# Kernel tuning notes

Measured on AMD Instinct MI355X. Metric: run time of the kernel, lower is better.

The kernel has to match this reference:

```python
import jax, jax.numpy as jnp
import numpy as np


def setup_inputs() -> dict:
    key = jax.random.key(0)
    ks = jax.random.split(key, 5)
    B, T, in_dim, out_dim = 8, 1024, 4096, 4096
    b_in, b_out, bs_in, bs_out, rank = 16, 16, 256, 256, 128
    std = np.sqrt(0.02).astype(np.float32)
    x = jax.random.normal(ks[0], (B, T, in_dim), dtype=jnp.float32)
    S = jax.random.uniform(ks[1], (b_out, b_in, rank), dtype=jnp.float32)
    U = std * jax.random.normal(ks[2], (b_out, rank, bs_out), dtype=jnp.float32)
    Vt = std * jax.random.normal(ks[3], (b_in, bs_in, rank), dtype=jnp.float32)
    bias = jax.random.normal(ks[4], (out_dim,), dtype=jnp.float32)
    return {"x": x, "S": S, "U": U, "Vt": Vt, "bias": bias}


def _blast_weight(S, U, Vt, in_dim):
    # Faithful to AbstractBlast.weight(eye(in_dim)): pass identity through the
    # block low-rank chain to materialize the dense weight W (in_dim, out_dim).
    b_in, bs_in, rank = Vt.shape
    I = jnp.eye(in_dim, dtype=Vt.dtype)
    # xp: (b_in, in_dim, bs_in) -- block-column slices of the identity
    xp = I.reshape(in_dim, b_in, bs_in).transpose(1, 0, 2)
    y = jnp.einsum('jms,jsr->jmr', xp, Vt)     # (b_in, in_dim, rank)
    z = jnp.einsum('jmr,ojr->omr', y, S)        # (b_out, in_dim, rank)
    out = jnp.einsum('omr,orp->omp', z, U)      # (b_out, in_dim, bs_out)
    W = out.transpose(1, 0, 2).reshape(in_dim, -1)  # (in_dim, out_dim)
    return W


def reference(x, S, U, Vt, bias):
    in_dim = x.shape[-1]
    X = x.reshape(-1, in_dim)                   # to2D
    W = _blast_weight(S, U, Vt, in_dim)
    out = bias + X @ W                          # addmm
    return out.reshape(*x.shape[:-1], -1)       # undo_to2D
```

## Files before the change

kernel.cpp:

```cpp
#include <hip/hip_runtime.h>
#include <hip/hip_bf16.h>


typedef __bf16 bf16x8 __attribute__((ext_vector_type(8)));
typedef __bf16 bf16x4 __attribute__((ext_vector_type(4)));
typedef float  f32x4  __attribute__((ext_vector_type(4)));

#define IN_DIM  4096
#define OUT_DIM 4096
#define NROWS   8192
#define BJ      16
#define BO      16
#define RANK    128

__device__ __forceinline__ bf16x4 cvt4(f32x4 v) {
  bf16x4 r;
  r[0] = (__bf16)v[0]; r[1] = (__bf16)v[1]; r[2] = (__bf16)v[2]; r[3] = (__bf16)v[3];
  return r;
}
__device__ __forceinline__ f32x4 lo4(bf16x8 v) {
  return (f32x4){(float)v[0], (float)v[1], (float)v[2], (float)v[3]};
}
__device__ __forceinline__ f32x4 hi4(bf16x8 v) {
  return (f32x4){(float)v[4], (float)v[5], (float)v[6], (float)v[7]};
}

__global__ __launch_bounds__(256) void prep_frag(
    const float* __restrict__ Vt, const float* __restrict__ U,
    __bf16* __restrict__ vtf, __bf16* __restrict__ utf)
{
  const int NV = BJ * 256 * RANK;
  int v = blockIdx.x * 256 + threadIdx.x;
  if (v < NV) {
    const int e = v & 7, lane = (v >> 3) & 63, ks = (v >> 9) & 7,
              rf = (v >> 12) & 7, j = v >> 15;
    const int l = lane & 15, lh = lane >> 4;
    const int s = ks * 32 + lh * 8 + e, r = rf * 16 + l;
    vtf[v] = (__bf16)Vt[((size_t)(j * 256 + s)) * RANK + r];
  } else {
    const int u = v - NV;
    const int e = u & 7, lane = (u >> 3) & 63, ks = (u >> 9) & 3,
              pf = (u >> 11) & 15, o = u >> 15;
    const int l = lane & 15, lh = lane >> 4;
    const int r = ks * 32 + lh * 8 + e, p = pf * 16 + l;
    utf[u] = (__bf16)U[((size_t)(o * RANK + r)) * 256 + p];
  }
}

__global__ __launch_bounds__(256, 4) void k1_T(
    const float* __restrict__ x, const __bf16* __restrict__ vtf,
    __bf16* __restrict__ T)
{
  __shared__ __bf16 X_lds[64 * 256];

  const int tid  = threadIdx.x;
  const int lane = tid & 63;
  const int w    = tid >> 6;
  const int l15  = lane & 15;
  const int lhi  = lane >> 4;
  const int b    = blockIdx.x;
  const int j    = (b >> 3) & 15;
  const int mt   = (b & 7) * 16 + (b >> 7);
  const size_t rowbase = (size_t)mt * 64;

  #pragma unroll
  for (int i = 0; i < 16; ++i) {
    const int row = w * 16 + i;
    const f32x4 v = __builtin_nontemporal_load(
        (const f32x4*)(x + (rowbase + row) * IN_DIM + j * 256 + lane * 4));
    const int c = (lane >> 1) ^ (row & 15);
    *(bf16x4*)&X_lds[row * 256 + c * 8 + (lane & 1) * 4] = cvt4(v);
  }
  __syncthreads();

  f32x4 acc[2][4];
  #pragma unroll
  for (int a = 0; a < 2; ++a)
    #pragma unroll
    for (int c = 0; c < 4; ++c) acc[a][c] = (f32x4){0.f, 0.f, 0.f, 0.f};

  const __bf16* va = vtf + ((size_t)(j * 8 + w * 2) * 8) * 512 + lane * 8;
  #pragma unroll
  for (int ks = 0; ks < 8; ++ks) {
    bf16x8 bfr[4];
    #pragma unroll
    for (int nf = 0; nf < 4; ++nf) {
      const int c = (ks * 4 + lhi) ^ l15;
      bfr[nf] = *(const bf16x8*)&X_lds[(nf * 16 + l15) * 256 + c * 8];
    }
    const bf16x8 a0 = *(const bf16x8*)(va + (size_t)ks * 512);
    const bf16x8 a1 = *(const bf16x8*)(va + (size_t)(8 + ks) * 512);
    #pragma unroll
    for (int nf = 0; nf < 4; ++nf) {
      acc[0][nf] = __builtin_amdgcn_mfma_f32_16x16x32_bf16(a0, bfr[nf], acc[0][nf], 0, 0, 0);
      acc[1][nf] = __builtin_amdgcn_mfma_f32_16x16x32_bf16(a1, bfr[nf], acc[1][nf], 0, 0, 0);
    }
  }
  #pragma unroll
  for (int rfi = 0; rfi < 2; ++rfi)
    #pragma unroll
    for (int nf = 0; nf < 4; ++nf) {
      *(bf16x4*)&T[((size_t)j * NROWS + rowbase + nf * 16 + l15) * RANK
                   + (w * 2 + rfi) * 16 + lhi * 4] = cvt4(acc[rfi][nf]);
    }
}

__global__ __launch_bounds__(256, 4) void k2_fused(
    const __bf16* __restrict__ T, const float* __restrict__ S,
    const __bf16* __restrict__ utf, const float* __restrict__ bias,
    float* __restrict__ out)
{
  __shared__ float  S_lds[BJ * RANK];
  __shared__ __bf16 u_lds[64 * RANK];

  const int tid = threadIdx.x;
  const int b   = blockIdx.x;
  const int o   = (b >> 3) & 15;
  const int mt  = (b & 7) * 16 + (b >> 7);
  const size_t rowbase = (size_t)mt * 64;

  {
    const float* sb = S + (size_t)o * (BJ * RANK);
    #pragma unroll
    for (int h = 0; h < 2; ++h) {
      const int idx = tid + h * 256;
      *(f32x4*)&S_lds[idx * 4] = *(const f32x4*)(sb + idx * 4);
    }
  }
  __syncthreads();

  {
    const int nb = tid >> 4;
    const int rs = tid & 15;
    const __bf16* tg = T + (rowbase + nb * 4) * RANK + rs * 8;
    const size_t jstride = (size_t)NROWS * RANK;
    f32x4 uac[4][2];
    #pragma unroll
    for (int i = 0; i < 4; ++i) {
      uac[i][0] = (f32x4){0.f, 0.f, 0.f, 0.f};
      uac[i][1] = (f32x4){0.f, 0.f, 0.f, 0.f};
    }

    #pragma unroll 4
    for (int jb = 0; jb < BJ; ++jb) {
      const __bf16* tj = tg + (size_t)jb * jstride;
      bf16x8 tv[4];
      #pragma unroll
      for (int i = 0; i < 4; ++i) tv[i] = *(const bf16x8*)(tj + i * RANK);
      const float* sj = &S_lds[jb * RANK + rs * 8];
      const f32x4 s0 = *(const f32x4*)(sj);
      const f32x4 s1 = *(const f32x4*)(sj + 4);
      #pragma unroll
      for (int i = 0; i < 4; ++i) {
        uac[i][0] = s0 * lo4(tv[i]) + uac[i][0];
        uac[i][1] = s1 * hi4(tv[i]) + uac[i][1];
      }
    }
    #pragma unroll
    for (int i = 0; i < 4; ++i) {
      const int n = nb * 4 + i;
      bf16x8 uw;
      const f32x4 a = uac[i][0], bb = uac[i][1];
      uw[0]=(__bf16)a[0];  uw[1]=(__bf16)a[1];  uw[2]=(__bf16)a[2];  uw[3]=(__bf16)a[3];
      uw[4]=(__bf16)bb[0]; uw[5]=(__bf16)bb[1]; uw[6]=(__bf16)bb[2]; uw[7]=(__bf16)bb[3];
      const int swz = rs ^ (n & 15);
      *(bf16x8*)&u_lds[n * RANK + swz * 8] = uw;
    }
  }
  __syncthreads();

  {
    const int lane = tid & 63;
    const int w    = tid >> 6;
    const int l15  = lane & 15;
    const int lhi  = lane >> 4;

    f32x4 acc[4][4];
    #pragma unroll
    for (int a = 0; a < 4; ++a)
      #pragma unroll
      for (int c = 0; c < 4; ++c) acc[a][c] = (f32x4){0.f, 0.f, 0.f, 0.f};

    #pragma unroll
    for (int ks = 0; ks < 4; ++ks) {
      bf16x8 ubf[4];
      #pragma unroll
      for (int nf = 0; nf < 4; ++nf) {
        const int swz = (ks * 4 + lhi) ^ l15;
        ubf[nf] = *(const bf16x8*)&u_lds[(nf * 16 + l15) * RANK + swz * 8];
      }
      #pragma unroll
      for (int pi = 0; pi < 4; ++pi) {
        const bf16x8 af = *(const bf16x8*)(
            utf + ((size_t)((o * 16 + w * 4 + pi) * 4 + ks)) * 512 + lane * 8);
        #pragma unroll
        for (int nf = 0; nf < 4; ++nf)
          acc[pi][nf] = __builtin_amdgcn_mfma_f32_16x16x32_bf16(af, ubf[nf], acc[pi][nf], 0, 0, 0);
      }
    }

    #pragma unroll
    for (int pi = 0; pi < 4; ++pi) {
      const int colb = o * 256 + (w * 4 + pi) * 16 + lhi * 4;
      const f32x4 bv = *(const f32x4*)(bias + colb);
      #pragma unroll
      for (int nf = 0; nf < 4; ++nf) {
        __builtin_nontemporal_store(acc[pi][nf] + bv,
            (f32x4*)(out + (rowbase + nf * 16 + l15) * OUT_DIM + colb));
      }
    }
  }
}

extern "C" void kernel_launch(void* const* d_in, const int* in_sizes, int n_in,
                              void* d_out, int out_size, void* d_ws, size_t ws_size,
                              hipStream_t stream) {
  const float* x    = (const float*)d_in[0];
  const float* S    = (const float*)d_in[1];
  const float* U    = (const float*)d_in[2];
  const float* Vt   = (const float*)d_in[3];
  const float* bias = (const float*)d_in[4];
  float* out = (float*)d_out;

  __bf16* vtf = (__bf16*)d_ws;
  __bf16* utf = vtf + (size_t)BJ * 8 * 8 * 512;
  __bf16* T   = utf + (size_t)BO * 16 * 4 * 512;

  prep_frag<<<(2 * 524288) / 256, 256, 0, stream>>>(Vt, U, vtf, utf);
  k1_T<<<(NROWS / 64) * BJ, 256, 0, stream>>>(x, vtf, T);
  k2_fused<<<(NROWS / 64) * BO, 256, 0, stream>>>(T, S, utf, bias, out);
}
```

Baseline: 99.66 us.

## Transpose weight fragments through LDS and read S directly from global

The single scalar-gather prep kernel is split into two kernels, one for Vt and one for U. Each stages a coalesced float4 tile in padded shared memory and writes bf16x8 MFMA fragments, replacing the strided per-element global reads. The fused second kernel now reads S straight from global memory instead of staging it in LDS. That drops one barrier and 8KB of LDS per block, at the cost of repeated global or cache reads of S.

Measured after the change: 103.7 us. 1.04x slower.

```diff
diff --git a/kernel.cpp b/kernel.cpp
--- a/kernel.cpp
+++ b/kernel.cpp
@@ -25,25 +25,69 @@
   return (f32x4){(float)v[4], (float)v[5], (float)v[6], (float)v[7]};
 }
 
-__global__ __launch_bounds__(256) void prep_frag(
-    const float* __restrict__ Vt, const float* __restrict__ U,
-    __bf16* __restrict__ vtf, __bf16* __restrict__ utf)
-{
-  const int NV = BJ * 256 * RANK;
-  int v = blockIdx.x * 256 + threadIdx.x;
-  if (v < NV) {
-    const int e = v & 7, lane = (v >> 3) & 63, ks = (v >> 9) & 7,
-              rf = (v >> 12) & 7, j = v >> 15;
-    const int l = lane & 15, lh = lane >> 4;
-    const int s = ks * 32 + lh * 8 + e, r = rf * 16 + l;
-    vtf[v] = (__bf16)Vt[((size_t)(j * 256 + s)) * RANK + r];
-  } else {
-    const int u = v - NV;
-    const int e = u & 7, lane = (u >> 3) & 63, ks = (u >> 9) & 3,
-              pf = (u >> 11) & 15, o = u >> 15;
-    const int l = lane & 15, lh = lane >> 4;
-    const int r = ks * 32 + lh * 8 + e, p = pf * 16 + l;
-    utf[u] = (__bf16)U[((size_t)(o * RANK + r)) * 256 + p];
+__global__ __launch_bounds__(256) void prep_vtf(
+    const float* __restrict__ Vt, __bf16* __restrict__ vtf)
+{
+  __shared__ float t[32 * 129];
+  const int tid = threadIdx.x;
+  const int j   = blockIdx.x >> 3;
+  const int ks  = blockIdx.x & 7;
+
+  #pragma unroll
+  for (int it = 0; it < 4; ++it) {
+    const int c  = tid + it * 256;
+    const int sr = c >> 5, r4 = c & 31;
+    const f32x4 v = *(const f32x4*)(Vt + ((size_t)(j * 256 + ks * 32 + sr)) * RANK + r4 * 4);
+    t[sr * 129 + r4 * 4 + 0] = v[0];
+    t[sr * 129 + r4 * 4 + 1] = v[1];
+    t[sr * 129 + r4 * 4 + 2] = v[2];
+    t[sr * 129 + r4 * 4 + 3] = v[3];
+  }
+  __syncthreads();
+
+  const int lane = tid & 63;
+  const int l = lane & 15, lh = lane >> 4;
+  #pragma unroll
+  for (int h = 0; h < 2; ++h) {
+    const int rf = (tid >> 6) + h * 4;
+    bf16x8 o8;
+    #pragma unroll
+    for (int e = 0; e < 8; ++e)
+      o8[e] = (__bf16)t[(lh * 8 + e) * 129 + rf * 16 + l];
+    *(bf16x8*)&vtf[(((size_t)(j * 8 + rf) * 8 + ks) * 64 + lane) * 8] = o8;
+  }
+}
+
+__global__ __launch_bounds__(256) void prep_utf(
+    const float* __restrict__ U, __bf16* __restrict__ utf)
+{
+  __shared__ float t[32 * 257];
+  const int tid = threadIdx.x;
+  const int o   = blockIdx.x >> 2;
+  const int ks  = blockIdx.x & 3;
+
+  #pragma unroll
+  for (int it = 0; it < 8; ++it) {
+    const int c  = tid + it * 256;
+    const int rr = c >> 6, p4 = c & 63;
+    const f32x4 v = *(const f32x4*)(U + ((size_t)(o * RANK + ks * 32 + rr)) * 256 + p4 * 4);
+    t[rr * 257 + p4 * 4 + 0] = v[0];
+    t[rr * 257 + p4 * 4 + 1] = v[1];
+    t[rr * 257 + p4 * 4 + 2] = v[2];
+    t[rr * 257 + p4 * 4 + 3] = v[3];
+  }
+  __syncthreads();
+
+  const int lane = tid & 63;
+  const int l = lane & 15, lh = lane >> 4;
+  #pragma unroll
+  for (int h = 0; h < 4; ++h) {
+    const int pf = (tid >> 6) + h * 4;
+    bf16x8 o8;
+    #pragma unroll
+    for (int e = 0; e < 8; ++e)
+      o8[e] = (__bf16)t[(lh * 8 + e) * 257 + pf * 16 + l];
+    *(bf16x8*)&utf[(((size_t)(o * 16 + pf) * 4 + ks) * 64 + lane) * 8] = o8;
   }
 }
 
@@ -110,7 +154,6 @@
     const __bf16* __restrict__ utf, const float* __restrict__ bias,
     float* __restrict__ out)
 {
-  __shared__ float  S_lds[BJ * RANK];
   __shared__ __bf16 u_lds[64 * RANK];
 
   const int tid = threadIdx.x;
@@ -120,19 +163,10 @@
   const size_t rowbase = (size_t)mt * 64;
 
   {
-    const float* sb = S + (size_t)o * (BJ * RANK);
-    #pragma unroll
-    for (int h = 0; h < 2; ++h) {
-      const int idx = tid + h * 256;
-      *(f32x4*)&S_lds[idx * 4] = *(const f32x4*)(sb + idx * 4);
-    }
-  }
-  __syncthreads();
-
-  {
     const int nb = tid >> 4;
     const int rs = tid & 15;
     const __bf16* tg = T + (rowbase + nb * 4) * RANK + rs * 8;
+    const float*  sp = S + (size_t)o * (BJ * RANK) + rs * 8;
     const size_t jstride = (size_t)NROWS * RANK;
     f32x4 uac[4][2];
     #pragma unroll
@@ -147,9 +181,8 @@
       bf16x8 tv[4];
       #pragma unroll
       for (int i = 0; i < 4; ++i) tv[i] = *(const bf16x8*)(tj + i * RANK);
-      const float* sj = &S_lds[jb * RANK + rs * 8];
-      const f32x4 s0 = *(const f32x4*)(sj);
-      const f32x4 s1 = *(const f32x4*)(sj + 4);
+      const f32x4 s0 = *(const f32x4*)(sp + jb * RANK);
+      const f32x4 s1 = *(const f32x4*)(sp + jb * RANK + 4);
       #pragma unroll
       for (int i = 0; i < 4; ++i) {
         uac[i][0] = s0 * lo4(tv[i]) + uac[i][0];
@@ -226,7 +259,8 @@
   __bf16* utf = vtf + (size_t)BJ * 8 * 8 * 512;
   __bf16* T   = utf + (size_t)BO * 16 * 4 * 512;
 
-  prep_frag<<<(2 * 524288) / 256, 256, 0, stream>>>(Vt, U, vtf, utf);
+  prep_vtf<<<BJ * 8, 256, 0, stream>>>(Vt, vtf);
+  prep_utf<<<BO * 4, 256, 0, stream>>>(U, utf);
   k1_T<<<(NROWS / 64) * BJ, 256, 0, stream>>>(x, vtf, T);
   k2_fused<<<(NROWS / 64) * BO, 256, 0, stream>>>(T, S, utf, bias, out);
 }
```
